# Kernel tuning notes

Hardware: AMD Instinct MI355X
Metric: run time of the kernel (lower is better)

## Reference

```python
import jax, jax.numpy as jnp
import numpy as np

B, R, L, E = 64, 36, 64, 512
LAMBDA_SOFTMAX = 9.0
NORM_EPS = 1e-12   # F.normalize eps
COS_EPS = 1e-8     # F.cosine_similarity eps


def _l2norm(x):
    return x / jnp.maximum(jnp.linalg.norm(x, axis=-1, keepdims=True), NORM_EPS)


def setup_inputs() -> dict:
    key = jax.random.key(0)
    k1, k2, k3 = jax.random.split(key, 3)
    images = jax.random.normal(k1, (B, R, E), dtype=jnp.float32)
    captions = jax.random.normal(k2, (B, L, E), dtype=jnp.float32)
    cap_lens = jax.random.randint(k3, (B,), 1, L + 1, dtype=jnp.int32)
    return {"images": images, "captions": captions, "cap_lens": cap_lens}


def reference(images, captions, cap_lens):
    # images: (B_img, R, E) region features; captions: (B_cap, L, E) token features
    img = _l2norm(images)
    cap = _l2norm(captions)

    # pairwise token-to-region similarity: (cap, img, L, R)
    sim = jnp.einsum('cle,ire->cilr', cap, img)
    # softmax over regions with temperature lambda_softmax.
    # NOTE: the original masks padded TOKEN rows with -inf before this softmax,
    # but those rows' outputs are fully zeroed below, so skipping the -inf fill
    # is mathematically equivalent (and NaN-free).
    attn_w = jax.nn.softmax(LAMBDA_SOFTMAX * sim, axis=-1)
    # attended image vector per (caption, image, token): (cap, img, L, E)
    attn = jnp.einsum('cilr,ire->cile', attn_w, img)

    # cosine similarity over feature dim
    dot = jnp.einsum('cle,cile->cil', cap, attn)
    na = jnp.linalg.norm(cap, axis=-1)[:, None, :]   # (cap, 1, L)
    nb = jnp.linalg.norm(attn, axis=-1)              # (cap, img, L)
    r = dot / jnp.maximum(na * nb, COS_EPS)          # (cap, img, L)

    # zero out padded tokens, then mean over the full padded length L
    valid = (jnp.arange(L)[None, :] < cap_lens[:, None]).astype(r.dtype)  # (cap, L)
    r = r * valid[:, None, :]
    sim_scores = r.mean(axis=-1)  # (cap, img)
    return sim_scores
```

## Files before the change

### kernel.cpp

```cpp
#include <hip/hip_runtime.h>
#include <stdint.h>

#define NCAP 64
#define NIMG 64
#define LTOK 64
#define RREG 36
#define EDIM 512
#define LAM 9.0f
#define SSTR 38

#define IMGT_STRIDE 18432

#define CHUNK_BYTES 34816
#define LDS_BYTES 38912

typedef __attribute__((ext_vector_type(8))) short bf16x8;
typedef __attribute__((ext_vector_type(4))) float f32x4;
typedef __attribute__((ext_vector_type(8))) unsigned short u16x8;

typedef const __attribute__((address_space(1))) void* gas1_t;
typedef __attribute__((address_space(3))) void* las3_t;

__device__ __forceinline__ void gl16(const void* g, void* l) {
  __builtin_amdgcn_global_load_lds((gas1_t)g, (las3_t)l, 16, 0, 0);
}

__device__ __forceinline__ unsigned short f2bf(float f) {
  unsigned int u = __float_as_uint(f);
  u += 0x7FFFu + ((u >> 16) & 1u);
  return (unsigned short)(u >> 16);
}

__global__ __launch_bounds__(256) void k_prep(const float* __restrict__ cap,
                                              const float* __restrict__ img,
                                              unsigned short* __restrict__ capT,
                                              unsigned short* __restrict__ imgT,
                                              float* __restrict__ G2) {
  __shared__ __align__(16) char gfr[49152];
  int tid = threadIdx.x;
  int w = tid >> 6, lane = tid & 63;
  int bid = blockIdx.x;

  if (bid < 64) {
    int i = bid;
    for (int t = tid; t < 1024; t += 256) {
      if ((t & 15) >= 4) {
        u16x8 z = {};
        *(u16x8*)(gfr + 32768 + t * 16) = z;
      }
    }
    int kk = lane >> 2, kg = lane & 3;
#pragma unroll
    for (int t = 0; t < 9; ++t) {
      int r = w + t * 4;
      const float* p = img + ((size_t)i * RREG + r) * EDIM + lane * 8;
      float4 a = *(const float4*)p;
      float4 b = *(const float4*)(p + 4);
      float ss = a.x * a.x + a.y * a.y + a.z * a.z + a.w * a.w +
                 b.x * b.x + b.y * b.y + b.z * b.z + b.w * b.w;
#pragma unroll
      for (int off = 1; off < 64; off <<= 1) ss += __shfl_xor(ss, off);
      float sc = 1.0f / fmaxf(sqrtf(ss), 1e-12f);
      u16x8 o = {f2bf(a.x * sc), f2bf(a.y * sc), f2bf(a.z * sc),
                 f2bf(a.w * sc), f2bf(b.x * sc), f2bf(b.y * sc),
                 f2bf(b.z * sc), f2bf(b.w * sc)};
      *(u16x8*)(gfr + (r >> 4) * 16384 + kk * 1024 +
                ((kg << 4) + (r & 15)) * 16) = o;
    }
    __syncthreads();
    if (w < 3) {
      f32x4 acc3[3];
#pragma unroll
      for (int n = 0; n < 3; ++n) acc3[n] = 0.f;
#pragma unroll
      for (int k2 = 0; k2 < 16; ++k2) {
        bf16x8 av = *(const bf16x8*)(gfr + w * 16384 + k2 * 1024 + lane * 16);
        bf16x8 b0 = *(const bf16x8*)(gfr + 0 * 16384 + k2 * 1024 + lane * 16);
        bf16x8 b1 = *(const bf16x8*)(gfr + 1 * 16384 + k2 * 1024 + lane * 16);
        bf16x8 b2 = *(const bf16x8*)(gfr + 2 * 16384 + k2 * 1024 + lane * 16);
        acc3[0] = __builtin_amdgcn_mfma_f32_16x16x32_bf16(av, b0, acc3[0], 0, 0, 0);
        acc3[1] = __builtin_amdgcn_mfma_f32_16x16x32_bf16(av, b1, acc3[1], 0, 0, 0);
        acc3[2] = __builtin_amdgcn_mfma_f32_16x16x32_bf16(av, b2, acc3[2], 0, 0, 0);
      }
      int rq = lane & 15, kgq = lane >> 4;
#pragma unroll
      for (int n = 0; n < 3; ++n)
#pragma unroll
        for (int j = 0; j < 4; ++j) {
          int R = w * 16 + kgq * 4 + j, C = n * 16 + rq;
          if (R < RREG && C < RREG) {
            float v = acc3[n][j];
            G2[(size_t)i * 1296 + R * 36 + C] = (R == C) ? v : 2.0f * v;
          }
        }
    }
    return;
  }

  int kkw = lane >> 2, kgw = lane & 3;
  int v = (bid - 64) * 4 + w;
  const float* p;
  unsigned short* dst;
  if (v < NCAP * LTOK) {
    int c = v >> 6, row = v & 63;
    int m = row >> 4, rqw = row & 15;
    p = cap + (size_t)v * EDIM + lane * 8;
    dst = capT + (size_t)c * 32768 +
          (size_t)(((m * 16 + kkw) * 64 + kgw * 16 + rqw) * 8);
  } else {
    int vi = v - NCAP * LTOK;
    int i = vi / RREG;
    int r = vi - i * RREG;
    p = img + ((size_t)i * RREG + r) * EDIM + lane * 8;
    if (r < 32) {
      int n = r >> 4, rqw = r & 15;
      dst = imgT + (size_t)i * IMGT_STRIDE +
            (size_t)(((n * 16 + kkw) * 64 + kgw * 16 + rqw) * 8);
    } else {
      int rq2 = r - 32;
      dst = imgT + (size_t)i * IMGT_STRIDE + 16384 +
            (size_t)(kkw * 128 + (kgw * 4 + rq2) * 8);
    }
  }
  float4 a = *(const float4*)p;
  float4 b = *(const float4*)(p + 4);
  float ss = a.x * a.x + a.y * a.y + a.z * a.z + a.w * a.w +
             b.x * b.x + b.y * b.y + b.z * b.z + b.w * b.w;
#pragma unroll
  for (int off = 1; off < 64; off <<= 1) ss += __shfl_xor(ss, off);
  float sc = 1.0f / fmaxf(sqrtf(ss), 1e-12f);
  u16x8 o = {f2bf(a.x * sc), f2bf(a.y * sc), f2bf(a.z * sc), f2bf(a.w * sc),
             f2bf(b.x * sc), f2bf(b.y * sc), f2bf(b.z * sc), f2bf(b.w * sc)};
  *(u16x8*)dst = o;
}

__device__ __forceinline__ void stage_chunk(const unsigned short* capT,
                                            const unsigned short* imgT,
                                            char* buf, int c0, int i0, int ch,
                                            int w, int lane) {
#pragma unroll
  for (int j = 0; j < 5; ++j) {
    int t = w + j * 8;
    if (t < 16) {
      int wcap = t >> 3, m = (t >> 1) & 3, kk = t & 1;
      const unsigned short* src =
          capT + (size_t)(c0 + wcap) * 32768 +
          (size_t)((m * 16 + ch * 2 + kk) * 512) + lane * 8;
      gl16(src, buf + (wcap * 8 + m * 2 + kk) * 1024);
    } else if (t < 32) {
      int u = t - 16;
      int kk = u >> 3, i = (u >> 1) & 3, f = u & 1;
      const unsigned short* src =
          imgT + (size_t)(i0 + i) * IMGT_STRIDE +
          (size_t)((f * 16 + ch * 2 + kk) * 512) + lane * 8;
      gl16(src, buf + 16384 + ((kk * 4 + i) * 2 + f) * 1024);
    } else if (t < 34) {
      int kk = t - 32;
      const unsigned short* src =
          imgT + (size_t)(i0 + (lane >> 4)) * IMGT_STRIDE + 16384 +
          (ch * 2 + kk) * 128 + (lane & 15) * 8;
      gl16(src, buf + 32768 + kk * 1024);
    }
  }
}

__global__ __launch_bounds__(512, 4) void k_main(
    const unsigned short* __restrict__ capT,
    const unsigned short* __restrict__ imgT, const float* __restrict__ G2,
    const int* __restrict__ lens, float* __restrict__ out) {
  __shared__ __align__(16) char lds[LDS_BYTES];
  int tid = threadIdx.x;
  int w = tid >> 6, lane = tid & 63;
  int wc = w >> 2, wi = w & 3;
  int rq = lane & 15, kg = lane >> 4;
  int bid = blockIdx.x;
  int b = (bid & 7) * 64 + (bid >> 3);
  int cg = b >> 4, ig = b & 15;
  int c0 = cg * 2, i0 = ig * 4;

  f32x4 acc[4][3];
#pragma unroll
  for (int m = 0; m < 4; ++m)
#pragma unroll
    for (int n = 0; n < 3; ++n) acc[m][n] = 0.f;

  stage_chunk(capT, imgT, lds, c0, i0, 0, w, lane);
  __syncthreads();
#pragma unroll
  for (int ch = 0; ch < 8; ++ch) {
    char* cur = lds;
#pragma unroll
    for (int kk = 0; kk < 2; ++kk) {
      bf16x8 a0 = *(const bf16x8*)(cur + (wc * 8 + 0 * 2 + kk) * 1024 + lane * 16);
      bf16x8 a1 = *(const bf16x8*)(cur + (wc * 8 + 1 * 2 + kk) * 1024 + lane * 16);
      bf16x8 a2 = *(const bf16x8*)(cur + (wc * 8 + 2 * 2 + kk) * 1024 + lane * 16);
      bf16x8 a3 = *(const bf16x8*)(cur + (wc * 8 + 3 * 2 + kk) * 1024 + lane * 16);
      bf16x8 b0 = *(const bf16x8*)(cur + 16384 + ((kk * 4 + wi) * 2 + 0) * 1024 + lane * 16);
      bf16x8 b1 = *(const bf16x8*)(cur + 16384 + ((kk * 4 + wi) * 2 + 1) * 1024 + lane * 16);
      bf16x8 b2 = *(const bf16x8*)(cur + 32768 + kk * 1024 + wi * 256 +
                                   (kg * 4 + (rq & 3)) * 16);

      acc[0][0] = __builtin_amdgcn_mfma_f32_16x16x32_bf16(a0, b0, acc[0][0], 0, 0, 0);
      acc[0][1] = __builtin_amdgcn_mfma_f32_16x16x32_bf16(a0, b1, acc[0][1], 0, 0, 0);
      acc[0][2] = __builtin_amdgcn_mfma_f32_16x16x32_bf16(a0, b2, acc[0][2], 0, 0, 0);
      acc[1][0] = __builtin_amdgcn_mfma_f32_16x16x32_bf16(a1, b0, acc[1][0], 0, 0, 0);
      acc[1][1] = __builtin_amdgcn_mfma_f32_16x16x32_bf16(a1, b1, acc[1][1], 0, 0, 0);
      acc[1][2] = __builtin_amdgcn_mfma_f32_16x16x32_bf16(a1, b2, acc[1][2], 0, 0, 0);
      acc[2][0] = __builtin_amdgcn_mfma_f32_16x16x32_bf16(a2, b0, acc[2][0], 0, 0, 0);
      acc[2][1] = __builtin_amdgcn_mfma_f32_16x16x32_bf16(a2, b1, acc[2][1], 0, 0, 0);
      acc[2][2] = __builtin_amdgcn_mfma_f32_16x16x32_bf16(a2, b2, acc[2][2], 0, 0, 0);
      acc[3][0] = __builtin_amdgcn_mfma_f32_16x16x32_bf16(a3, b0, acc[3][0], 0, 0, 0);
      acc[3][1] = __builtin_amdgcn_mfma_f32_16x16x32_bf16(a3, b1, acc[3][1], 0, 0, 0);
      acc[3][2] = __builtin_amdgcn_mfma_f32_16x16x32_bf16(a3, b2, acc[3][2], 0, 0, 0);
    }
    __syncthreads();
    if (ch < 7) {
      stage_chunk(capT, imgT, lds, c0, i0, ch + 1, w, lane);
      __syncthreads();
    }
  }

  float* Sf = (float*)lds;
  int c = c0 + wc;
  int i = i0 + wi;
  int iu = __builtin_amdgcn_readfirstlane(i);
  const float* Gi = G2 + (size_t)iu * 1296;
  int len = lens[c];

#pragma unroll
  for (int pass = 0; pass < 2; ++pass) {
    bool mine = (wc == pass);
    int slot = wi;
    if (mine) {
#pragma unroll
      for (int m = 0; m < 4; ++m)
#pragma unroll
        for (int n = 0; n < 3; ++n)
#pragma unroll
          for (int j = 0; j < 4; ++j)
            if (n < 2 || rq < 4)
              Sf[(slot * 64 + m * 16 + kg * 4 + j) * SSTR + n * 16 + rq] =
                  acc[m][n][j];
    }
    __syncthreads();
    if (mine) {
      const float* Srow = Sf + (size_t)(slot * 64 + lane) * SSTR;
      float s[36];
#pragma unroll
      for (int r2 = 0; r2 < 18; ++r2) {
        float2 x = *(const float2*)(Srow + r2 * 2);
        s[r2 * 2 + 0] = x.x;
        s[r2 * 2 + 1] = x.y;
      }
      float mx = s[0];
#pragma unroll
      for (int r = 1; r < 36; ++r) mx = fmaxf(mx, s[r]);
      float p[36];
      float sum = 0.f, dotp = 0.f;
#pragma unroll
      for (int r = 0; r < 36; ++r) {
        p[r] = __expf(LAM * (s[r] - mx));
        sum += p[r];
        dotp = fmaf(p[r], s[r], dotp);
      }
      float q2 = 0.f;
#pragma unroll
      for (int r2 = 0; r2 < 36; ++r2) {
        float t = 0.f;
#pragma unroll
        for (int r = 0; r <= r2; ++r) t = fmaf(Gi[r2 * 36 + r], p[r], t);
        q2 = fmaf(t, p[r2], q2);
      }
      float inv = 1.0f / sum;
      float dn = dotp * inv;
      float nb = sqrtf(fmaxf(q2, 0.f)) * inv;
      float rcos = dn / fmaxf(nb, 1e-8f);
      float val = (lane < len) ? rcos : 0.f;
#pragma unroll
      for (int off = 1; off < 64; off <<= 1) val += __shfl_xor(val, off);
      if (lane == 0) out[c * 64 + i] = val * (1.0f / 64.0f);
    }
    if (pass == 0) __syncthreads();
  }
}

extern "C" void kernel_launch(void* const* d_in, const int* in_sizes, int n_in,
                              void* d_out, int out_size, void* d_ws,
                              size_t ws_size, hipStream_t stream) {
  const float* images = (const float*)d_in[0];
  const float* captions = (const float*)d_in[1];
  const int* lens = (const int*)d_in[2];
  float* out = (float*)d_out;

  char* ws = (char*)d_ws;
  unsigned short* capT = (unsigned short*)ws;
  unsigned short* imgT = (unsigned short*)(ws + 4194304);
  float* G = (float*)(ws + 4194304 + 2359296);

  k_prep<<<1664, 256, 0, stream>>>(captions, images, capT, imgT, G);
  k_main<<<512, 512, 0, stream>>>(capT, imgT, G, lens, out);
}
```

Measured before the change: 46.57 us.

## Split K across wave halves, one caption per block, double grid

Each block now handles one caption and four images instead of two captions. The two wave groups each compute half of the K dimension, and their partial similarity tiles are summed in LDS. The softmax/cosine epilogue is spread across all 8 waves at 32 tokens each, and per-half sums are reduced through a small LDS buffer. The grid doubles to 1024 blocks for more parallelism, at the cost of caption data no longer being shared across waves and an extra LDS accumulate pass with barriers.

```diff
diff --git a/kernel.cpp b/kernel.cpp
--- a/kernel.cpp
+++ b/kernel.cpp
@@ -11,8 +11,8 @@
 
 #define IMGT_STRIDE 18432
 
-#define CHUNK_BYTES 34816
-#define LDS_BYTES 38912
+#define CHUNK_BYTES 26624
+#define LDS_BYTES 38976
 
 typedef __attribute__((ext_vector_type(8))) short bf16x8;
 typedef __attribute__((ext_vector_type(4))) float f32x4;
@@ -136,30 +136,30 @@
 
 __device__ __forceinline__ void stage_chunk(const unsigned short* capT,
                                             const unsigned short* imgT,
-                                            char* buf, int c0, int i0, int ch,
+                                            char* buf, int c, int i0, int ch,
                                             int w, int lane) {
 #pragma unroll
-  for (int j = 0; j < 5; ++j) {
+  for (int j = 0; j < 4; ++j) {
     int t = w + j * 8;
-    if (t < 16) {
-      int wcap = t >> 3, m = (t >> 1) & 3, kk = t & 1;
+    if (t < 8) {
+      int m = t >> 1, khs = t & 1;
       const unsigned short* src =
-          capT + (size_t)(c0 + wcap) * 32768 +
-          (size_t)((m * 16 + ch * 2 + kk) * 512) + lane * 8;
-      gl16(src, buf + (wcap * 8 + m * 2 + kk) * 1024);
-    } else if (t < 32) {
-      int u = t - 16;
-      int kk = u >> 3, i = (u >> 1) & 3, f = u & 1;
+          capT + (size_t)c * 32768 +
+          (size_t)((m * 16 + khs * 8 + ch) * 512) + lane * 8;
+      gl16(src, buf + t * 1024);
+    } else if (t < 24) {
+      int u = t - 8;
+      int khs = u >> 3, img = (u >> 1) & 3, n = u & 1;
       const unsigned short* src =
-          imgT + (size_t)(i0 + i) * IMGT_STRIDE +
-          (size_t)((f * 16 + ch * 2 + kk) * 512) + lane * 8;
-      gl16(src, buf + 16384 + ((kk * 4 + i) * 2 + f) * 1024);
-    } else if (t < 34) {
-      int kk = t - 32;
+          imgT + (size_t)(i0 + img) * IMGT_STRIDE +
+          (size_t)((n * 16 + khs * 8 + ch) * 512) + lane * 8;
+      gl16(src, buf + 8192 + u * 1024);
+    } else if (t < 26) {
+      int khs = t - 24;
       const unsigned short* src =
           imgT + (size_t)(i0 + (lane >> 4)) * IMGT_STRIDE + 16384 +
-          (ch * 2 + kk) * 128 + (lane & 15) * 8;
-      gl16(src, buf + 32768 + kk * 1024);
+          (khs * 8 + ch) * 128 + (lane & 15) * 8;
+      gl16(src, buf + 24576 + khs * 1024);
     }
   }
 }
@@ -171,12 +171,12 @@
   __shared__ __align__(16) char lds[LDS_BYTES];
   int tid = threadIdx.x;
   int w = tid >> 6, lane = tid & 63;
-  int wc = w >> 2, wi = w & 3;
+  int wi = w & 3, kh = w >> 2;
   int rq = lane & 15, kg = lane >> 4;
   int bid = blockIdx.x;
-  int b = (bid & 7) * 64 + (bid >> 3);
-  int cg = b >> 4, ig = b & 15;
-  int c0 = cg * 2, i0 = ig * 4;
+  int b = (bid & 7) * 128 + (bid >> 3);
+  int c = b >> 4;
+  int i0 = (b & 15) * 4;
 
   f32x4 acc[4][3];
 #pragma unroll
@@ -184,104 +184,116 @@
 #pragma unroll
     for (int n = 0; n < 3; ++n) acc[m][n] = 0.f;
 
-  stage_chunk(capT, imgT, lds, c0, i0, 0, w, lane);
+  int aoff = kh * 1024 + lane * 16;
+  int boff = 8192 + (kh * 8 + wi * 2) * 1024 + lane * 16;
+  int qoff = 24576 + kh * 1024 + wi * 256 + (kg * 4 + (rq & 3)) * 16;
+
+  stage_chunk(capT, imgT, lds, c, i0, 0, w, lane);
   __syncthreads();
 #pragma unroll
   for (int ch = 0; ch < 8; ++ch) {
-    char* cur = lds;
-#pragma unroll
-    for (int kk = 0; kk < 2; ++kk) {
-      bf16x8 a0 = *(const bf16x8*)(cur + (wc * 8 + 0 * 2 + kk) * 1024 + lane * 16);
-      bf16x8 a1 = *(const bf16x8*)(cur + (wc * 8 + 1 * 2 + kk) * 1024 + lane * 16);
-      bf16x8 a2 = *(const bf16x8*)(cur + (wc * 8 + 2 * 2 + kk) * 1024 + lane * 16);
-      bf16x8 a3 = *(const bf16x8*)(cur + (wc * 8 + 3 * 2 + kk) * 1024 + lane * 16);
-      bf16x8 b0 = *(const bf16x8*)(cur + 16384 + ((kk * 4 + wi) * 2 + 0) * 1024 + lane * 16);
-      bf16x8 b1 = *(const bf16x8*)(cur + 16384 + ((kk * 4 + wi) * 2 + 1) * 1024 + lane * 16);
-      bf16x8 b2 = *(const bf16x8*)(cur + 32768 + kk * 1024 + wi * 256 +
-                                   (kg * 4 + (rq & 3)) * 16);
-
-      acc[0][0] = __builtin_amdgcn_mfma_f32_16x16x32_bf16(a0, b0, acc[0][0], 0, 0, 0);
-      acc[0][1] = __builtin_amdgcn_mfma_f32_16x16x32_bf16(a0, b1, acc[0][1], 0, 0, 0);
-      acc[0][2] = __builtin_amdgcn_mfma_f32_16x16x32_bf16(a0, b2, acc[0][2], 0, 0, 0);
-      acc[1][0] = __builtin_amdgcn_mfma_f32_16x16x32_bf16(a1, b0, acc[1][0], 0, 0, 0);
-      acc[1][1] = __builtin_amdgcn_mfma_f32_16x16x32_bf16(a1, b1, acc[1][1], 0, 0, 0);
-      acc[1][2] = __builtin_amdgcn_mfma_f32_16x16x32_bf16(a1, b2, acc[1][2], 0, 0, 0);
-      acc[2][0] = __builtin_amdgcn_mfma_f32_16x16x32_bf16(a2, b0, acc[2][0], 0, 0, 0);
-      acc[2][1] = __builtin_amdgcn_mfma_f32_16x16x32_bf16(a2, b1, acc[2][1], 0, 0, 0);
-      acc[2][2] = __builtin_amdgcn_mfma_f32_16x16x32_bf16(a2, b2, acc[2][2], 0, 0, 0);
-      acc[3][0] = __builtin_amdgcn_mfma_f32_16x16x32_bf16(a3, b0, acc[3][0], 0, 0, 0);
-      acc[3][1] = __builtin_amdgcn_mfma_f32_16x16x32_bf16(a3, b1, acc[3][1], 0, 0, 0);
-      acc[3][2] = __builtin_amdgcn_mfma_f32_16x16x32_bf16(a3, b2, acc[3][2], 0, 0, 0);
-    }
+    bf16x8 a0 = *(const bf16x8*)(lds + aoff + 0 * 2048);
+    bf16x8 a1 = *(const bf16x8*)(lds + aoff + 1 * 2048);
+    bf16x8 a2 = *(const bf16x8*)(lds + aoff + 2 * 2048);
+    bf16x8 a3 = *(const bf16x8*)(lds + aoff + 3 * 2048);
+    bf16x8 b0 = *(const bf16x8*)(lds + boff + 0 * 1024);
+    bf16x8 b1 = *(const bf16x8*)(lds + boff + 1 * 1024);
+    bf16x8 b2 = *(const bf16x8*)(lds + qoff);
+
+    acc[0][0] = __builtin_amdgcn_mfma_f32_16x16x32_bf16(a0, b0, acc[0][0], 0, 0, 0);
+    acc[0][1] = __builtin_amdgcn_mfma_f32_16x16x32_bf16(a0, b1, acc[0][1], 0, 0, 0);
+    acc[0][2] = __builtin_amdgcn_mfma_f32_16x16x32_bf16(a0, b2, acc[0][2], 0, 0, 0);
+    acc[1][0] = __builtin_amdgcn_mfma_f32_16x16x32_bf16(a1, b0, acc[1][0], 0, 0, 0);
+    acc[1][1] = __builtin_amdgcn_mfma_f32_16x16x32_bf16(a1, b1, acc[1][1], 0, 0, 0);
+    acc[1][2] = __builtin_amdgcn_mfma_f32_16x16x32_bf16(a1, b2, acc[1][2], 0, 0, 0);
+    acc[2][0] = __builtin_amdgcn_mfma_f32_16x16x32_bf16(a2, b0, acc[2][0], 0, 0, 0);
+    acc[2][1] = __builtin_amdgcn_mfma_f32_16x16x32_bf16(a2, b1, acc[2][1], 0, 0, 0);
+    acc[2][2] = __builtin_amdgcn_mfma_f32_16x16x32_bf16(a2, b2, acc[2][2], 0, 0, 0);
+    acc[3][0] = __builtin_amdgcn_mfma_f32_16x16x32_bf16(a3, b0, acc[3][0], 0, 0, 0);
+    acc[3][1] = __builtin_amdgcn_mfma_f32_16x16x32_bf16(a3, b1, acc[3][1], 0, 0, 0);
+    acc[3][2] = __builtin_amdgcn_mfma_f32_16x16x32_bf16(a3, b2, acc[3][2], 0, 0, 0);
+
     __syncthreads();
     if (ch < 7) {
-      stage_chunk(capT, imgT, lds, c0, i0, ch + 1, w, lane);
+      stage_chunk(capT, imgT, lds, c, i0, ch + 1, w, lane);
       __syncthreads();
     }
   }
 
   float* Sf = (float*)lds;
-  int c = c0 + wc;
+  float* part = (float*)(lds + 38912);
   int i = i0 + wi;
   int iu = __builtin_amdgcn_readfirstlane(i);
   const float* Gi = G2 + (size_t)iu * 1296;
   int len = lens[c];
 
-#pragma unroll
-  for (int pass = 0; pass < 2; ++pass) {
-    bool mine = (wc == pass);
-    int slot = wi;
-    if (mine) {
-#pragma unroll
-      for (int m = 0; m < 4; ++m)
-#pragma unroll
-        for (int n = 0; n < 3; ++n)
-#pragma unroll
-          for (int j = 0; j < 4; ++j)
-            if (n < 2 || rq < 4)
-              Sf[(slot * 64 + m * 16 + kg * 4 + j) * SSTR + n * 16 + rq] =
-                  acc[m][n][j];
-    }
-    __syncthreads();
-    if (mine) {
-      const float* Srow = Sf + (size_t)(slot * 64 + lane) * SSTR;
-      float s[36];
-#pragma unroll
-      for (int r2 = 0; r2 < 18; ++r2) {
-        float2 x = *(const float2*)(Srow + r2 * 2);
-        s[r2 * 2 + 0] = x.x;
-        s[r2 * 2 + 1] = x.y;
-      }
-      float mx = s[0];
-#pragma unroll
-      for (int r = 1; r < 36; ++r) mx = fmaxf(mx, s[r]);
-      float p[36];
-      float sum = 0.f, dotp = 0.f;
-#pragma unroll
-      for (int r = 0; r < 36; ++r) {
-        p[r] = __expf(LAM * (s[r] - mx));
-        sum += p[r];
-        dotp = fmaf(p[r], s[r], dotp);
-      }
-      float q2 = 0.f;
-#pragma unroll
-      for (int r2 = 0; r2 < 36; ++r2) {
-        float t = 0.f;
-#pragma unroll
-        for (int r = 0; r <= r2; ++r) t = fmaf(Gi[r2 * 36 + r], p[r], t);
-        q2 = fmaf(t, p[r2], q2);
-      }
-      float inv = 1.0f / sum;
-      float dn = dotp * inv;
-      float nb = sqrtf(fmaxf(q2, 0.f)) * inv;
-      float rcos = dn / fmaxf(nb, 1e-8f);
-      float val = (lane < len) ? rcos : 0.f;
-#pragma unroll
-      for (int off = 1; off < 64; off <<= 1) val += __shfl_xor(val, off);
-      if (lane == 0) out[c * 64 + i] = val * (1.0f / 64.0f);
-    }
-    if (pass == 0) __syncthreads();
-  }
+  if (kh == 0) {
+#pragma unroll
+    for (int m = 0; m < 4; ++m)
+#pragma unroll
+      for (int n = 0; n < 3; ++n)
+#pragma unroll
+        for (int j = 0; j < 4; ++j)
+          if (n < 2 || rq < 4)
+            Sf[(wi * 64 + m * 16 + kg * 4 + j) * SSTR + n * 16 + rq] =
+                acc[m][n][j];
+  }
+  __syncthreads();
+  if (kh == 1) {
+#pragma unroll
+    for (int m = 0; m < 4; ++m)
+#pragma unroll
+      for (int n = 0; n < 3; ++n)
+#pragma unroll
+        for (int j = 0; j < 4; ++j)
+          if (n < 2 || rq < 4) {
+            int idx = (wi * 64 + m * 16 + kg * 4 + j) * SSTR + n * 16 + rq;
+            Sf[idx] += acc[m][n][j];
+          }
+  }
+  __syncthreads();
+
+  if (lane < 32) {
+    int tok = kh * 32 + lane;
+    const float* Srow = Sf + (size_t)(wi * 64 + tok) * SSTR;
+    float s[36];
+#pragma unroll
+    for (int r2 = 0; r2 < 18; ++r2) {
+      float2 x = *(const float2*)(Srow + r2 * 2);
+      s[r2 * 2 + 0] = x.x;
+      s[r2 * 2 + 1] = x.y;
+    }
+    float mx = s[0];
+#pragma unroll
+    for (int r = 1; r < 36; ++r) mx = fmaxf(mx, s[r]);
+    float p[36];
+    float sum = 0.f, dotp = 0.f;
+#pragma unroll
+    for (int r = 0; r < 36; ++r) {
+      p[r] = __expf(LAM * (s[r] - mx));
+      sum += p[r];
+      dotp = fmaf(p[r], s[r], dotp);
+    }
+    float q2 = 0.f;
+#pragma unroll
+    for (int r2 = 0; r2 < 36; ++r2) {
+      float t = 0.f;
+#pragma unroll
+      for (int r = 0; r <= r2; ++r) t = fmaf(Gi[r2 * 36 + r], p[r], t);
+      q2 = fmaf(t, p[r2], q2);
+    }
+    float inv = 1.0f / sum;
+    float dn = dotp * inv;
+    float nb = sqrtf(fmaxf(q2, 0.f)) * inv;
+    float rcos = dn / fmaxf(nb, 1e-8f);
+    float val = (tok < len) ? rcos : 0.f;
+#pragma unroll
+    for (int off = 1; off < 32; off <<= 1) val += __shfl_xor(val, off);
+    if (lane == 0) part[wi * 2 + kh] = val;
+  }
+  __syncthreads();
+  if (tid < 4)
+    out[c * 64 + i0 + tid] = (part[tid * 2] + part[tid * 2 + 1]) * (1.0f / 64.0f);
 }
 
 extern "C" void kernel_launch(void* const* d_in, const int* in_sizes, int n_in,
@@ -298,5 +310,5 @@
   float* G = (float*)(ws + 4194304 + 2359296);
 
   k_prep<<<1664, 256, 0, stream>>>(captions, images, capT, imgT, G);
-  k_main<<<512, 512, 0, stream>>>(capT, imgT, G, lens, out);
-}
+  k_main<<<1024, 512, 0, stream>>>(capT, imgT, G, lens, out);
+}
```

After: 59.01 us. 26.7% more time.
